# Kernel optimization log

Measured on AMD Instinct MI355X. Metric: run time of the kernel, lower is better.

The kernel has to match this reference:

```python
import jax, jax.numpy as jnp
import numpy as np

N = 100000   # nodes
IN = 128     # in_size
OUT = 64     # out_size (== out_size * layer_num_heads, heads=1)
P = 3        # meta-paths
E = 1600000  # edges per meta-path graph
HID = 32     # semantic attention hidden size


def setup_inputs() -> dict:
    key = jax.random.key(0)
    ks = jax.random.split(key, 8)
    h = jax.random.normal(ks[0], (N, IN), dtype=jnp.float32)
    edge_src = jax.random.randint(ks[1], (P, E), 0, N)
    edge_dst = jax.random.randint(ks[2], (P, E), 0, N)
    # xavier_uniform-style init for linear weights
    def xavier(k, shape):
        fan_in, fan_out = shape[0], shape[1]
        lim = np.sqrt(6.0 / (fan_in + fan_out)).astype(np.float32)
        return jax.random.uniform(k, shape, jnp.float32, -lim, lim)
    gc_w = xavier(ks[3], (IN, OUT))
    gc_b = jnp.zeros((OUT,), jnp.float32)
    sa_w1 = xavier(ks[4], (OUT, HID))
    sa_b1 = jnp.zeros((HID,), jnp.float32)
    sa_w2 = xavier(ks[5], (HID, 1))
    return {"h": h, "gc_w": gc_w, "gc_b": gc_b, "sa_w1": sa_w1,
            "sa_b1": sa_b1, "sa_w2": sa_w2,
            "edge_src": edge_src, "edge_dst": edge_dst}


def _graph_conv(h, gc_w, gc_b, src, dst):
    # DGL GraphConv, norm='both', activation=relu, allow_zero_in_degree.
    ones = jnp.ones(src.shape, h.dtype)
    out_deg = jax.ops.segment_sum(ones, src, num_segments=N)
    in_deg = jax.ops.segment_sum(ones, dst, num_segments=N)
    norm_src = jax.lax.rsqrt(jnp.maximum(out_deg, 1.0))  # [N]
    norm_dst = jax.lax.rsqrt(jnp.maximum(in_deg, 1.0))   # [N]
    # in_feats > out_feats: project first, then aggregate
    feat = (h * norm_src[:, None]) @ gc_w                # [N, OUT]
    agg = jax.ops.segment_sum(feat[src], dst, num_segments=N)  # [N, OUT]
    return jax.nn.relu(agg * norm_dst[:, None] + gc_b)


def reference(h, gc_w, gc_b, sa_w1, sa_b1, sa_w2, edge_src, edge_dst):
    # shared GraphConv applied to each meta-path graph (dropout p=0 -> identity)
    embs = [_graph_conv(h, gc_w, gc_b, edge_src[p], edge_dst[p]) for p in range(P)]
    z = jnp.stack(embs, axis=1)                          # [N, P, OUT]
    # semantic attention: small MLP -> mean over nodes -> softmax over meta-paths
    w = jnp.tanh(z @ sa_w1 + sa_b1) @ sa_w2              # [N, P, 1]
    beta = jax.nn.softmax(w.mean(axis=0), axis=0)        # [P, 1]
    out = (beta[None, :, :] * z).sum(axis=1)             # [N, OUT]
    return out, z
```

## Files before the change

### kernel.cpp

```cpp
#include <hip/hip_runtime.h>

#define NN 100000
#define IN_F 128
#define OUT_F 64
#define PP 3
#define EE 1600000
#define TOT (PP * EE)
#define HID 32
#define SEG_N (PP * NN)
#define NC1024 98
#define NCB (NC1024 * PP)
#define CAPC 19456
#define CAPS 21504
#define CHUNK 8192
#define NSX ((EE + CHUNK - 1) / CHUNK)
#define LCAP 64
#define NFB (NCB * 32)
#define WSLOTS 256

__device__ __forceinline__ unsigned short f2bf(float f) {
    unsigned u = __float_as_uint(f);
    u += 0x7FFFu + ((u >> 16) & 1u);
    return (unsigned short)(u >> 16);
}
__device__ __forceinline__ float bf2f(unsigned short b) {
    return __uint_as_float((unsigned)b << 16);
}
__device__ __forceinline__ float tanh_fast(float x) {
    float ax = fabsf(x);
    float e = __expf(-2.f * ax);
    float t = (1.f - e) / (1.f + e);
    return copysignf(t, x);
}

__global__ void scatter_sortd(const int* __restrict__ src, const int* __restrict__ dst,
                              unsigned* __restrict__ gcur_d, unsigned* __restrict__ gbuf_d) {
    __shared__ unsigned sorted[CHUNK];
    __shared__ unsigned hist4[4][NC1024];
    __shared__ unsigned pre[NC1024 + 1];
    __shared__ unsigned wcur[4][NC1024];
    __shared__ unsigned gbase[NC1024];
    int tid = threadIdx.x, wv = tid >> 6;
    int p = blockIdx.y;
    for (int i = tid; i < 4 * NC1024; i += 256) hist4[i / NC1024][i % NC1024] = 0u;
    __syncthreads();
    int e0 = blockIdx.x * CHUNK;
    const int* sp = src + (size_t)p * EE;
    const int* dp = dst + (size_t)p * EE;
    for (int i = 0; i < CHUNK / 256; ++i) {
        int e = e0 + i * 256 + tid;
        if (e < EE) atomicAdd(&hist4[wv][dp[e] >> 10], 1u);
    }
    __syncthreads();
    if (tid == 0) {
        unsigned a = 0;
        for (int b = 0; b < NC1024; ++b) {
            pre[b] = a;
            a += hist4[0][b] + hist4[1][b] + hist4[2][b] + hist4[3][b];
        }
        pre[NC1024] = a;
    }
    __syncthreads();
    if (tid < NC1024) {
        unsigned a = pre[tid];
        wcur[0][tid] = a; a += hist4[0][tid];
        wcur[1][tid] = a; a += hist4[1][tid];
        wcur[2][tid] = a; a += hist4[2][tid];
        wcur[3][tid] = a; a += hist4[3][tid];
        unsigned tt = a - pre[tid];
        gbase[tid] = tt ? atomicAdd(&gcur_d[tid * PP + p], (tt + 15u) & ~15u) : 0u;
    }
    __syncthreads();
    for (int i = 0; i < CHUNK / 256; ++i) {
        int e = e0 + i * 256 + tid;
        if (e < EE) {
            int s = sp[e], d = dp[e];
            unsigned pos = atomicAdd(&wcur[wv][(unsigned)d >> 10], 1u);
            sorted[pos] = (unsigned)s | ((unsigned)(d & 1023) << 17);
        }
    }
    __syncthreads();
    for (int b = 0; b < NC1024; ++b) {
        unsigned st = pre[b], len = pre[b + 1] - st;
        if (!len) continue;
        unsigned padded = (len + 15u) & ~15u;
        unsigned gb = gbase[b];
        size_t gout = (size_t)(b * PP + p) * CAPC;
        for (unsigned j = tid; j < padded; j += 256)
            if (gb + j < CAPC)
                gbuf_d[gout + gb + j] = (j < len) ? sorted[st + j] : 0xFFFFFFFFu;
    }
}

__global__ void scatter_sorts(const int* __restrict__ src,
                              unsigned* __restrict__ gcur_s, unsigned short* __restrict__ gbuf_s) {
    __shared__ unsigned short sorted[CHUNK];
    __shared__ unsigned hist4[4][NC1024];
    __shared__ unsigned pre[NC1024 + 1];
    __shared__ unsigned wcur[4][NC1024];
    __shared__ unsigned gbase[NC1024];
    int tid = threadIdx.x, wv = tid >> 6;
    int p = blockIdx.y;
    for (int i = tid; i < 4 * NC1024; i += 256) hist4[i / NC1024][i % NC1024] = 0u;
    __syncthreads();
    int e0 = blockIdx.x * CHUNK;
    const int* sp = src + (size_t)p * EE;
    for (int i = 0; i < CHUNK / 256; ++i) {
        int e = e0 + i * 256 + tid;
        if (e < EE) atomicAdd(&hist4[wv][sp[e] >> 10], 1u);
    }
    __syncthreads();
    if (tid == 0) {
        unsigned a = 0;
        for (int b = 0; b < NC1024; ++b) {
            pre[b] = a;
            a += hist4[0][b] + hist4[1][b] + hist4[2][b] + hist4[3][b];
        }
        pre[NC1024] = a;
    }
    __syncthreads();
    if (tid < NC1024) {
        unsigned a = pre[tid];
        wcur[0][tid] = a; a += hist4[0][tid];
        wcur[1][tid] = a; a += hist4[1][tid];
        wcur[2][tid] = a; a += hist4[2][tid];
        wcur[3][tid] = a; a += hist4[3][tid];
        unsigned tt = a - pre[tid];
        gbase[tid] = tt ? atomicAdd(&gcur_s[tid * PP + p], (tt + 31u) & ~31u) : 0u;
    }
    __syncthreads();
    for (int i = 0; i < CHUNK / 256; ++i) {
        int e = e0 + i * 256 + tid;
        if (e < EE) {
            int s = sp[e];
            unsigned pos = atomicAdd(&wcur[wv][(unsigned)s >> 10], 1u);
            sorted[pos] = (unsigned short)(s & 1023);
        }
    }
    __syncthreads();
    for (int b = 0; b < NC1024; ++b) {
        unsigned st = pre[b], len = pre[b + 1] - st;
        if (!len) continue;
        unsigned padded = (len + 31u) & ~31u;
        unsigned gb = gbase[b];
        size_t gout = (size_t)(b * PP + p) * CAPS;
        for (unsigned j = tid; j < padded; j += 256)
            if (gb + j < CAPS)
                gbuf_s[gout + gb + j] = (j < len) ? sorted[st + j] : (unsigned short)0xFFFFu;
    }
}

__global__ void src_hist(const unsigned* __restrict__ gcur_s, const unsigned short* __restrict__ gbuf_s,
                         float* __restrict__ nsrc) {
    __shared__ unsigned hist[4][1024];
    int tid = threadIdx.x;
    int wv = tid >> 6;
    for (int i = tid; i < 4 * 1024; i += 256) hist[i >> 10][i & 1023] = 0u;
    __syncthreads();
    int c = blockIdx.x;
    int blk = c / PP, p = c - blk * PP;
    unsigned cnt = gcur_s[c]; if (cnt > CAPS) cnt = CAPS;
    const unsigned short* gb = gbuf_s + (size_t)c * CAPS;
    for (unsigned j = tid; j < cnt; j += 256) {
        unsigned v = gb[j];
        if (v <= 1023u) atomicAdd(&hist[wv][v], 1u);
    }
    __syncthreads();
    for (int i = tid; i < 1024; i += 256) {
        int n = blk * 1024 + i;
        unsigned hv = hist[0][i] + hist[1][i] + hist[2][i] + hist[3][i];
        if (n < NN) nsrc[p * NN + n] = rsqrtf(fmaxf((float)hv, 1.f));
    }
}

__global__ void __launch_bounds__(256) proj_fused(const float* __restrict__ h,
                                                  const float* __restrict__ gc_w,
                                                  const float* __restrict__ nsrc,
                                                  unsigned short* __restrict__ t0,
                                                  unsigned short* __restrict__ t1,
                                                  unsigned short* __restrict__ t2) {
    __shared__ float w_lds[IN_F * OUT_F];
    __shared__ float h_lds[32 * IN_F];
    int tid = threadIdx.x;
    for (int i = tid; i < IN_F * OUT_F / 4; i += 256)
        ((float4*)w_lds)[i] = ((const float4*)gc_w)[i];
    size_t r0 = (size_t)blockIdx.x * 32;
    for (int i = tid; i < 32 * IN_F / 4; i += 256)
        ((float4*)h_lds)[i] = ((const float4*)(h + r0 * IN_F))[i];
    __syncthreads();
    int wave = tid >> 6, lane = tid & 63;
    float acc[8] = {0.f, 0.f, 0.f, 0.f, 0.f, 0.f, 0.f, 0.f};
    for (int k = 0; k < IN_F; k += 4) {
        float w0 = w_lds[k * OUT_F + lane];
        float w1 = w_lds[(k + 1) * OUT_F + lane];
        float w2 = w_lds[(k + 2) * OUT_F + lane];
        float w3 = w_lds[(k + 3) * OUT_F + lane];
#pragma unroll
        for (int r = 0; r < 8; ++r) {
            float4 hv = *(const float4*)&h_lds[(wave * 8 + r) * IN_F + k];
            acc[r] = fmaf(hv.x, w0, fmaf(hv.y, w1, fmaf(hv.z, w2, fmaf(hv.w, w3, acc[r]))));
        }
    }
#pragma unroll
    for (int r = 0; r < 8; ++r) {
        size_t n = r0 + wave * 8 + r;
        float a = acc[r];
        t0[n * OUT_F + lane] = f2bf(a * nsrc[n]);
        t1[n * OUT_F + lane] = f2bf(a * nsrc[NN + n]);
        t2[n * OUT_F + lane] = f2bf(a * nsrc[2 * NN + n]);
    }
}

__global__ void fine_split(const unsigned* __restrict__ gcur_d, unsigned* __restrict__ gbuf_d,
                           unsigned* __restrict__ foff, unsigned* __restrict__ fcnt) {
    __shared__ unsigned stage[CAPC];
    __shared__ unsigned hist[4][32], pre[32], cur[4][32];
    int c = blockIdx.x;
    int tid = threadIdx.x;
    int wv = tid >> 6;
    if (tid < 32) { hist[0][tid] = 0u; hist[1][tid] = 0u; hist[2][tid] = 0u; hist[3][tid] = 0u; }
    __syncthreads();
    unsigned cnt = gcur_d[c]; if (cnt > CAPC) cnt = CAPC;
    unsigned* gb = gbuf_d + (size_t)c * CAPC;
    for (unsigned j = tid; j < cnt; j += 256) {
        unsigned v = gb[j];
        stage[j] = v;
        if (v != 0xFFFFFFFFu) atomicAdd(&hist[wv][v >> 22], 1u);
    }
    __syncthreads();
    if (tid == 0) {
        unsigned a = 0;
        for (int i = 0; i < 32; ++i) {
            pre[i] = a;
            a += hist[0][i] + hist[1][i] + hist[2][i] + hist[3][i];
        }
    }
    __syncthreads();
    if (tid < 32) {
        unsigned a = pre[tid];
        cur[0][tid] = a; a += hist[0][tid];
        cur[1][tid] = a; a += hist[1][tid];
        cur[2][tid] = a; a += hist[2][tid];
        cur[3][tid] = a; a += hist[3][tid];
        foff[c * 32 + tid] = (unsigned)c * CAPC + pre[tid];
        fcnt[c * 32 + tid] = a - pre[tid];
    }
    __syncthreads();
    for (unsigned j = tid; j < cnt; j += 256) {
        unsigned v = stage[j];
        if (v == 0xFFFFFFFFu) continue;
        unsigned pos = atomicAdd(&cur[wv][v >> 22], 1u);
        gb[pos] = ((v & 0x1FFFFu) << 7) | ((v >> 17) & 31u);
    }
}

__global__ void __launch_bounds__(256, 8)
gather3d(const unsigned* __restrict__ foff, const unsigned* __restrict__ fcnt,
         const unsigned* __restrict__ gbuf_f,
         const unsigned short* __restrict__ t0, const unsigned short* __restrict__ t1,
         const unsigned short* __restrict__ t2,
         const float* __restrict__ gc_b, const float* __restrict__ sa_w1,
         const float* __restrict__ sa_b1, const float* __restrict__ sa_w2,
         float* __restrict__ zbuf, float* __restrict__ wsum) {
    __shared__ unsigned lists[32 * LCAP];
    __shared__ unsigned lcnt[32];
    __shared__ float zsh[4][OUT_F];
    int tid = threadIdx.x;
    int lane = tid & 63, wave = tid >> 6;
    int j = lane & 31, half = lane >> 5;
    unsigned w1p[16];
#pragma unroll
    for (int q = 0; q < 16; ++q) {
        float a = sa_w1[(half * 32 + 2 * q) * HID + j];
        float b = sa_w1[(half * 32 + 2 * q + 1) * HID + j];
        w1p[q] = (unsigned)f2bf(a) | ((unsigned)f2bf(b) << 16);
    }
    float b1r = sa_b1[j];
    float w2r = sa_w2[j];
    float bsr = gc_b[lane];
    if (tid < 32) lcnt[tid] = 0u;
    __syncthreads();

    int f = blockIdx.x;
    int c = f >> 5, sub = f & 31;
    int blk = c / PP, p = c - blk * PP;
    const char* tpc = (const char*)((p == 0) ? t0 : (p == 1) ? t1 : t2);
    unsigned l2 = (unsigned)(lane << 1);
    unsigned base = foff[f];
    unsigned cnt = fcnt[f];
    for (unsigned i = tid; i < cnt; i += 256) {
        unsigned v = gbuf_f[base + i];
        unsigned node = v & 31u;
        unsigned sl = atomicAdd(&lcnt[node], 1u);
        if (sl < LCAP) lists[node * LCAP + sl] = v & 0xFFFFFF80u;
    }
    __syncthreads();

    int nbase = blk * 1024 + sub * 32;
    float logacc = 0.f;
    for (int k = 0; k < 8; ++k) {
        int node = wave * 8 + k;
        int n = nbase + node;
        if (n >= NN) continue;
        unsigned ind = lcnt[node];
        unsigned c2 = ind < LCAP ? ind : LCAP;
        unsigned pl = lists[node * LCAP + lane];
        float acc = 0.f;
        unsigned i = 0;
        for (; i + 8 <= c2; i += 8) {
            unsigned o0 = (unsigned)__builtin_amdgcn_readlane((int)pl, (int)i);
            unsigned o1 = (unsigned)__builtin_amdgcn_readlane((int)pl, (int)i + 1);
            unsigned o2 = (unsigned)__builtin_amdgcn_readlane((int)pl, (int)i + 2);
            unsigned o3 = (unsigned)__builtin_amdgcn_readlane((int)pl, (int)i + 3);
            unsigned o4 = (unsigned)__builtin_amdgcn_readlane((int)pl, (int)i + 4);
            unsigned o5 = (unsigned)__builtin_amdgcn_readlane((int)pl, (int)i + 5);
            unsigned o6 = (unsigned)__builtin_amdgcn_readlane((int)pl, (int)i + 6);
            unsigned o7 = (unsigned)__builtin_amdgcn_readlane((int)pl, (int)i + 7);
            float p0 = bf2f(*(const unsigned short*)(tpc + (o0 + l2)));
            float p1 = bf2f(*(const unsigned short*)(tpc + (o1 + l2)));
            float p2 = bf2f(*(const unsigned short*)(tpc + (o2 + l2)));
            float p3 = bf2f(*(const unsigned short*)(tpc + (o3 + l2)));
            float p4 = bf2f(*(const unsigned short*)(tpc + (o4 + l2)));
            float p5 = bf2f(*(const unsigned short*)(tpc + (o5 + l2)));
            float p6 = bf2f(*(const unsigned short*)(tpc + (o6 + l2)));
            float p7 = bf2f(*(const unsigned short*)(tpc + (o7 + l2)));
            acc += ((p0 + p1) + (p2 + p3)) + ((p4 + p5) + (p6 + p7));
        }
        for (; i < c2; ++i) {
            unsigned o0 = (unsigned)__builtin_amdgcn_readlane((int)pl, (int)i);
            acc += bf2f(*(const unsigned short*)(tpc + (o0 + l2)));
        }
        float ndv = rsqrtf(fmaxf((float)ind, 1.f));
        float zv = fmaxf(fmaf(acc, ndv, bsr), 0.f);
        zbuf[((size_t)n * PP + p) * OUT_F + lane] = zv;
        zsh[wave][lane] = zv;
        float hp = 0.f;
        const float4* zrow = (const float4*)&zsh[wave][half * 32];
#pragma unroll
        for (int q = 0; q < 8; ++q) {
            float4 zq = zrow[q];
            unsigned u0 = w1p[2 * q], u1 = w1p[2 * q + 1];
            hp = fmaf(zq.x, __uint_as_float(u0 << 16), hp);
            hp = fmaf(zq.y, __uint_as_float(u0 & 0xFFFF0000u), hp);
            hp = fmaf(zq.z, __uint_as_float(u1 << 16), hp);
            hp = fmaf(zq.w, __uint_as_float(u1 & 0xFFFF0000u), hp);
        }
        hp += __shfl_xor(hp, 32);
        logacc += tanh_fast(hp + b1r) * w2r;
    }
#pragma unroll
    for (int off = 1; off < 64; off <<= 1) logacc += __shfl_xor(logacc, off);
    if (lane == 0) atomicAdd(&wsum[(blockIdx.x & (WSLOTS - 1)) * PP + p], logacc * 0.5f);
}

__global__ void beta_kernel(const float* __restrict__ wsum, float* __restrict__ beta) {
    if (threadIdx.x == 0) {
        float m[PP] = {0.f, 0.f, 0.f};
        for (int i = 0; i < WSLOTS; ++i)
            for (int p = 0; p < PP; ++p) m[p] += wsum[i * PP + p];
        float mx = -1e30f;
        for (int p = 0; p < PP; ++p) { m[p] *= (1.0f / NN); mx = fmaxf(mx, m[p]); }
        float e[PP], s = 0.f;
        for (int p = 0; p < PP; ++p) { e[p] = expf(m[p] - mx); s += e[p]; }
        for (int p = 0; p < PP; ++p) beta[p] = e[p] / s;
    }
}

__global__ void out_kernel(const float* __restrict__ zbuf, const float* __restrict__ beta,
                           float* __restrict__ out) {
    int t = blockIdx.x * 256 + threadIdx.x;
    if (t >= NN * (OUT_F / 4)) return;
    int n = t >> 4;
    int q = t & 15;
    float b0 = beta[0], b1 = beta[1], b2 = beta[2];
    const float4 v0 = ((const float4*)(zbuf + ((size_t)n * PP + 0) * OUT_F))[q];
    const float4 v1 = ((const float4*)(zbuf + ((size_t)n * PP + 1) * OUT_F))[q];
    const float4 v2 = ((const float4*)(zbuf + ((size_t)n * PP + 2) * OUT_F))[q];
    float4 r;
    r.x = b0 * v0.x + b1 * v1.x + b2 * v2.x;
    r.y = b0 * v0.y + b1 * v1.y + b2 * v2.y;
    r.z = b0 * v0.z + b1 * v1.z + b2 * v2.z;
    r.w = b0 * v0.w + b1 * v1.w + b2 * v2.w;
    ((float4*)out)[t] = r;
}

extern "C" void kernel_launch(void* const* d_in, const int* in_sizes, int n_in,
                              void* d_out, int out_size, void* d_ws, size_t ws_size,
                              hipStream_t stream) {
    const float* h     = (const float*)d_in[0];
    const float* gc_w  = (const float*)d_in[1];
    const float* gc_b  = (const float*)d_in[2];
    const float* sa_w1 = (const float*)d_in[3];
    const float* sa_b1 = (const float*)d_in[4];
    const float* sa_w2 = (const float*)d_in[5];
    const int* esrc    = (const int*)d_in[6];
    const int* edst    = (const int*)d_in[7];

    float* out  = (float*)d_out;
    float* zbuf = out + (size_t)NN * OUT_F;
    unsigned short* t0 = (unsigned short*)out;
    unsigned short* t1 = t0 + (size_t)NN * OUT_F;

    char* ws = (char*)d_ws;
    const size_t OFF_GBD  = 0;
    const size_t OFF_GBS  = 22900000;
    const size_t OFF_T2   = 22900000;
    const size_t OFF_NSRC = 35800000;
    const size_t OFF_FOFF = 37100000;
    const size_t OFF_FCNT = 37150000;
    const size_t OFF_GCD  = 37200000;
    const size_t OFF_GCS  = 37210000;
    const size_t OFF_WSUM = 37220000;
    const size_t OFF_BETA = 37230000;

    unsigned* gbuf_d       = (unsigned*)(ws + OFF_GBD);
    unsigned short* gbuf_s = (unsigned short*)(ws + OFF_GBS);
    unsigned short* t2     = (unsigned short*)(ws + OFF_T2);
    float* nsrc            = (float*)(ws + OFF_NSRC);
    unsigned* foff         = (unsigned*)(ws + OFF_FOFF);
    unsigned* fcnt         = (unsigned*)(ws + OFF_FCNT);
    unsigned* gcur_d       = (unsigned*)(ws + OFF_GCD);
    unsigned* gcur_s       = (unsigned*)(ws + OFF_GCS);
    float* wsum            = (float*)(ws + OFF_WSUM);
    float* beta            = (float*)(ws + OFF_BETA);

    hipMemsetAsync(gcur_d, 0, NCB * sizeof(unsigned), stream);
    hipMemsetAsync(gcur_s, 0, NCB * sizeof(unsigned), stream);
    hipMemsetAsync(wsum, 0, WSLOTS * PP * sizeof(float), stream);

    scatter_sortd<<<dim3(NSX, PP), 256, 0, stream>>>(esrc, edst, gcur_d, gbuf_d);
    scatter_sorts<<<dim3(NSX, PP), 256, 0, stream>>>(esrc, gcur_s, gbuf_s);
    src_hist<<<NCB, 256, 0, stream>>>(gcur_s, gbuf_s, nsrc);
    proj_fused<<<NN / 32, 256, 0, stream>>>(h, gc_w, nsrc, t0, t1, t2);
    fine_split<<<NCB, 256, 0, stream>>>(gcur_d, gbuf_d, foff, fcnt);
    gather3d<<<NFB, 256, 0, stream>>>(foff, fcnt, gbuf_d, t0, t1, t2,
                                      gc_b, sa_w1, sa_b1, sa_w2, zbuf, wsum);
    beta_kernel<<<1, 64, 0, stream>>>(wsum, beta);
    out_kernel<<<(NN * (OUT_F / 4) + 255) / 256, 256, 0, stream>>>(zbuf, beta, out);
}
```

Measured before the change: 402.3 us.

## Sort edges per destination node in fine_split to drop gather's LDS list build

fine_split now counts edges into 1024 per-node buckets instead of 32 sub-blocks. It prefix-scans them with a block-wide scan and writes a per-node offset and count. The gather kernel reads each node's edge list directly from global memory by offset, so it no longer rebuilds per-node lists in LDS with atomics. This trades a heavier fine_split (larger LDS histograms and a multi-step scan) for less atomic and LDS work in the gather kernel, and makes the foff/fcnt arrays larger.

```diff
diff --git a/kernel.cpp b/kernel.cpp
--- a/kernel.cpp
+++ b/kernel.cpp
@@ -14,7 +14,6 @@
 #define CAPS 21504
 #define CHUNK 8192
 #define NSX ((EE + CHUNK - 1) / CHUNK)
-#define LCAP 64
 #define NFB (NCB * 32)
 #define WSLOTS 256
 
@@ -214,56 +213,68 @@
 __global__ void fine_split(const unsigned* __restrict__ gcur_d, unsigned* __restrict__ gbuf_d,
                            unsigned* __restrict__ foff, unsigned* __restrict__ fcnt) {
     __shared__ unsigned stage[CAPC];
-    __shared__ unsigned hist[4][32], pre[32], cur[4][32];
+    __shared__ unsigned hist[4][1024];
+    __shared__ unsigned cur[4][1024];
+    __shared__ unsigned scan[256];
     int c = blockIdx.x;
     int tid = threadIdx.x;
     int wv = tid >> 6;
-    if (tid < 32) { hist[0][tid] = 0u; hist[1][tid] = 0u; hist[2][tid] = 0u; hist[3][tid] = 0u; }
+    for (int i = tid; i < 4 * 1024; i += 256) hist[i >> 10][i & 1023] = 0u;
     __syncthreads();
     unsigned cnt = gcur_d[c]; if (cnt > CAPC) cnt = CAPC;
     unsigned* gb = gbuf_d + (size_t)c * CAPC;
     for (unsigned j = tid; j < cnt; j += 256) {
         unsigned v = gb[j];
         stage[j] = v;
-        if (v != 0xFFFFFFFFu) atomicAdd(&hist[wv][v >> 22], 1u);
-    }
-    __syncthreads();
-    if (tid == 0) {
-        unsigned a = 0;
-        for (int i = 0; i < 32; ++i) {
-            pre[i] = a;
-            a += hist[0][i] + hist[1][i] + hist[2][i] + hist[3][i];
-        }
-    }
-    __syncthreads();
-    if (tid < 32) {
-        unsigned a = pre[tid];
-        cur[0][tid] = a; a += hist[0][tid];
-        cur[1][tid] = a; a += hist[1][tid];
-        cur[2][tid] = a; a += hist[2][tid];
-        cur[3][tid] = a; a += hist[3][tid];
-        foff[c * 32 + tid] = (unsigned)c * CAPC + pre[tid];
-        fcnt[c * 32 + tid] = a - pre[tid];
+        if (v != 0xFFFFFFFFu) atomicAdd(&hist[wv][(v >> 17) & 1023u], 1u);
+    }
+    __syncthreads();
+    unsigned t0h = hist[0][4 * tid]     + hist[1][4 * tid]     + hist[2][4 * tid]     + hist[3][4 * tid];
+    unsigned t1h = hist[0][4 * tid + 1] + hist[1][4 * tid + 1] + hist[2][4 * tid + 1] + hist[3][4 * tid + 1];
+    unsigned t2h = hist[0][4 * tid + 2] + hist[1][4 * tid + 2] + hist[2][4 * tid + 2] + hist[3][4 * tid + 2];
+    unsigned t3h = hist[0][4 * tid + 3] + hist[1][4 * tid + 3] + hist[2][4 * tid + 3] + hist[3][4 * tid + 3];
+    unsigned tsum = t0h + t1h + t2h + t3h;
+    unsigned x = tsum;
+    scan[tid] = x;
+    __syncthreads();
+    for (int off = 1; off < 256; off <<= 1) {
+        unsigned y = (tid >= off) ? scan[tid - off] : 0u;
+        __syncthreads();
+        x += y;
+        scan[tid] = x;
+        __syncthreads();
+    }
+    unsigned a = x - tsum;
+    unsigned gbase = (unsigned)c * CAPC;
+#pragma unroll
+    for (int q = 0; q < 4; ++q) {
+        int b = 4 * tid + q;
+        unsigned h0 = hist[0][b], h1 = hist[1][b], h2 = hist[2][b], h3 = hist[3][b];
+        foff[(size_t)c * 1024 + b] = gbase + a;
+        fcnt[(size_t)c * 1024 + b] = h0 + h1 + h2 + h3;
+        cur[0][b] = a; a += h0;
+        cur[1][b] = a; a += h1;
+        cur[2][b] = a; a += h2;
+        cur[3][b] = a; a += h3;
     }
     __syncthreads();
     for (unsigned j = tid; j < cnt; j += 256) {
         unsigned v = stage[j];
         if (v == 0xFFFFFFFFu) continue;
-        unsigned pos = atomicAdd(&cur[wv][v >> 22], 1u);
-        gb[pos] = ((v & 0x1FFFFu) << 7) | ((v >> 17) & 31u);
+        unsigned pos = atomicAdd(&cur[wv][(v >> 17) & 1023u], 1u);
+        gb[pos] = (v & 0x1FFFFu) << 7;
     }
 }
 
 __global__ void __launch_bounds__(256, 8)
-gather3d(const unsigned* __restrict__ foff, const unsigned* __restrict__ fcnt,
+gather3f(const unsigned* __restrict__ foff, const unsigned* __restrict__ fcnt,
          const unsigned* __restrict__ gbuf_f,
          const unsigned short* __restrict__ t0, const unsigned short* __restrict__ t1,
          const unsigned short* __restrict__ t2,
          const float* __restrict__ gc_b, const float* __restrict__ sa_w1,
          const float* __restrict__ sa_b1, const float* __restrict__ sa_w2,
          float* __restrict__ zbuf, float* __restrict__ wsum) {
-    __shared__ unsigned lists[32 * LCAP];
-    __shared__ unsigned lcnt[32];
+    __shared__ unsigned nfo[32], nfc[32];
     __shared__ float zsh[4][OUT_F];
     int tid = threadIdx.x;
     int lane = tid & 63, wave = tid >> 6;
@@ -278,21 +289,16 @@
     float b1r = sa_b1[j];
     float w2r = sa_w2[j];
     float bsr = gc_b[lane];
-    if (tid < 32) lcnt[tid] = 0u;
-    __syncthreads();
 
     int f = blockIdx.x;
     int c = f >> 5, sub = f & 31;
     int blk = c / PP, p = c - blk * PP;
     const char* tpc = (const char*)((p == 0) ? t0 : (p == 1) ? t1 : t2);
     unsigned l2 = (unsigned)(lane << 1);
-    unsigned base = foff[f];
-    unsigned cnt = fcnt[f];
-    for (unsigned i = tid; i < cnt; i += 256) {
-        unsigned v = gbuf_f[base + i];
-        unsigned node = v & 31u;
-        unsigned sl = atomicAdd(&lcnt[node], 1u);
-        if (sl < LCAP) lists[node * LCAP + sl] = v & 0xFFFFFF80u;
+    if (tid < 32) {
+        size_t g = (size_t)c * 1024 + sub * 32 + tid;
+        nfo[tid] = foff[g];
+        nfc[tid] = fcnt[g];
     }
     __syncthreads();
 
@@ -302,9 +308,9 @@
         int node = wave * 8 + k;
         int n = nbase + node;
         if (n >= NN) continue;
-        unsigned ind = lcnt[node];
-        unsigned c2 = ind < LCAP ? ind : LCAP;
-        unsigned pl = lists[node * LCAP + lane];
+        unsigned ind = nfc[node];
+        unsigned c2 = ind < 64u ? ind : 64u;
+        unsigned pl = gbuf_f[nfo[node] + lane];
         float acc = 0.f;
         unsigned i = 0;
         for (; i + 8 <= c2; i += 8) {
@@ -407,11 +413,11 @@
     const size_t OFF_T2   = 22900000;
     const size_t OFF_NSRC = 35800000;
     const size_t OFF_FOFF = 37100000;
-    const size_t OFF_FCNT = 37150000;
-    const size_t OFF_GCD  = 37200000;
-    const size_t OFF_GCS  = 37210000;
-    const size_t OFF_WSUM = 37220000;
-    const size_t OFF_BETA = 37230000;
+    const size_t OFF_FCNT = 38350000;
+    const size_t OFF_GCD  = 39600000;
+    const size_t OFF_GCS  = 39610000;
+    const size_t OFF_WSUM = 39620000;
+    const size_t OFF_BETA = 39630000;
 
     unsigned* gbuf_d       = (unsigned*)(ws + OFF_GBD);
     unsigned short* gbuf_s = (unsigned short*)(ws + OFF_GBS);
@@ -433,7 +439,7 @@
     src_hist<<<NCB, 256, 0, stream>>>(gcur_s, gbuf_s, nsrc);
     proj_fused<<<NN / 32, 256, 0, stream>>>(h, gc_w, nsrc, t0, t1, t2);
     fine_split<<<NCB, 256, 0, stream>>>(gcur_d, gbuf_d, foff, fcnt);
-    gather3d<<<NFB, 256, 0, stream>>>(foff, fcnt, gbuf_d, t0, t1, t2,
+    gather3f<<<NFB, 256, 0, stream>>>(foff, fcnt, gbuf_d, t0, t1, t2,
                                       gc_b, sa_w1, sa_b1, sa_w2, zbuf, wsum);
     beta_kernel<<<1, 64, 0, stream>>>(wsum, beta);
     out_kernel<<<(NN * (OUT_F / 4) + 255) / 256, 256, 0, stream>>>(zbuf, beta, out);
```

Result: slower. 439.5 us (+9.3%).
